# Performance work log

Measured on AMD Instinct MI355X. Metric: run time of the kernel, lower is better.

## Reference

```python
import jax, jax.numpy as jnp
import numpy as np

N_NODES = 50000
N_EDGES = 600000
IN_DIM, H_DIM, OUT_DIM = 128, 128, 64
NUM_RELS = 8


def setup_inputs() -> dict:
    key = jax.random.key(0)
    ks = jax.random.split(key, 10)
    x = jax.random.normal(ks[0], (N_NODES, IN_DIM), dtype=jnp.float32)
    edge_index = jax.random.randint(ks[1], (2, N_EDGES), 0, N_NODES, dtype=jnp.int64 if jax.config.read('jax_enable_x64') else jnp.int32)
    edge_type = jax.random.randint(ks[2], (N_EDGES,), 0, NUM_RELS, dtype=edge_index.dtype)
    s1 = 1.0 / np.sqrt(IN_DIM)
    s2 = 1.0 / np.sqrt(H_DIM)
    W1 = jax.random.uniform(ks[3], (NUM_RELS, IN_DIM, H_DIM), jnp.float32, -s1, s1)
    root1 = jax.random.uniform(ks[4], (IN_DIM, H_DIM), jnp.float32, -s1, s1)
    b1 = jnp.zeros((H_DIM,), jnp.float32)
    W2 = jax.random.uniform(ks[5], (NUM_RELS, H_DIM, OUT_DIM), jnp.float32, -s2, s2)
    root2 = jax.random.uniform(ks[6], (H_DIM, OUT_DIM), jnp.float32, -s2, s2)
    b2 = jnp.zeros((OUT_DIM,), jnp.float32)
    return {"x": x, "edge_index": edge_index, "edge_type": edge_type,
            "W1": W1, "root1": root1, "b1": b1, "W2": W2, "root2": root2, "b2": b2}


def rgcn_conv(x, src, dst, et, W, Wr, b, num_rels):
    # h_i = W_root x_i + b + sum_r (1/|N_r(i)|) sum_{j in N_r(i)} W_r x_j  (mean per relation)
    N = x.shape[0]
    xs = jnp.einsum('ni,rio->rno', x, W)          # [R, N, out]: transform once per relation
    msgs = xs[et, src]                            # [E, out]: gather per-edge transformed source
    seg = dst * num_rels + et                     # combined (dst, rel) segment id
    deg = jax.ops.segment_sum(jnp.ones(et.shape, jnp.float32), seg, num_segments=N * num_rels)
    norm = 1.0 / jnp.maximum(deg[seg], 1.0)       # per-relation in-degree normalization
    agg = jax.ops.segment_sum(msgs * norm[:, None], dst, num_segments=N)
    return agg + x @ Wr + b


def reference(x, edge_index, edge_type, W1, root1, b1, W2, root2, b2):
    src, dst = edge_index[0], edge_index[1]
    h = rgcn_conv(x, src, dst, edge_type, W1, root1, b1, NUM_RELS)
    h = jax.nn.relu(h)
    out = rgcn_conv(h, src, dst, edge_type, W2, root2, b2, NUM_RELS)
    return out
```

## Files before the change

kernel.cpp:

```cpp
#include <hip/hip_runtime.h>

#define NRELS 8

typedef __attribute__((ext_vector_type(8))) short short8;
typedef __attribute__((ext_vector_type(4))) float f32x4;

__device__ __forceinline__ unsigned short f2bf(float f) {
  unsigned int u = __float_as_uint(f);
  u += 0x7FFFu + ((u >> 16) & 1u);
  return (unsigned short)(u >> 16);
}
__device__ __forceinline__ float bf2f(unsigned short h) {
  return __uint_as_float(((unsigned int)h) << 16);
}

__device__ __forceinline__ void gload_lds16(const void* g, void* l) {
  __builtin_amdgcn_global_load_lds(
      (const __attribute__((address_space(1))) unsigned int*)g,
      (__attribute__((address_space(3))) unsigned int*)l, 16, 0, 0);
}


__global__ __launch_bounds__(256) void zero_kernel(int* __restrict__ p, int n) {
  int i = blockIdx.x * blockDim.x + threadIdx.x;
  if (i < n) p[i] = 0;
}


__global__ __launch_bounds__(256) void hist_kernel(
    const int* __restrict__ dstp, const int* __restrict__ et, int E,
    int* __restrict__ hist) {
  int i = blockIdx.x * blockDim.x + threadIdx.x;
  if (i < E) {
    atomicAdd(&hist[(size_t)dstp[i] * NRELS + et[i]], 1);
  }
}


__global__ __launch_bounds__(256) void scan1_kernel(
    const int* __restrict__ hist, int M, int* __restrict__ row_off,
    int* __restrict__ bsum, float* __restrict__ nrm) {
  __shared__ int s[256];
  int t = threadIdx.x;
  int i = blockIdx.x * 256 + t;
  int v = (i < M) ? hist[i] : 0;
  if (i < M) nrm[i] = 1.0f / (float)max(v, 1);
  s[t] = v;
  __syncthreads();
  for (int off = 1; off < 256; off <<= 1) {
    int u = (t >= off) ? s[t - off] : 0;
    __syncthreads();
    s[t] += u;
    __syncthreads();
  }
  if (i < M) row_off[i] = s[t] - v;
  if (t == 255) bsum[blockIdx.x] = s[255];
}

__global__ __launch_bounds__(256) void scan2_kernel(int* __restrict__ bsum, int NB) {
  __shared__ int s[256];
  int t = threadIdx.x;
  int C = (NB + 255) / 256;
  int b0 = t * C, b1 = min(NB, b0 + C);
  int sum = 0;
  for (int i = b0; i < b1; i++) sum += bsum[i];
  s[t] = sum;
  __syncthreads();
  for (int off = 1; off < 256; off <<= 1) {
    int u = (t >= off) ? s[t - off] : 0;
    __syncthreads();
    s[t] += u;
    __syncthreads();
  }
  int base = (t == 0) ? 0 : s[t - 1];
  for (int i = b0; i < b1; i++) {
    int v = bsum[i];
    bsum[i] = base;
    base += v;
  }
  if (t == 255) bsum[NB] = s[255];
}

__global__ __launch_bounds__(256) void scan3_kernel(
    int* __restrict__ row_off, int* __restrict__ cursor,
    const int* __restrict__ bsum, int M, int NB) {
  int i = blockIdx.x * 256 + threadIdx.x;
  if (i < M) {
    int v = row_off[i] + bsum[i >> 8];
    row_off[i] = v;
    cursor[i] = v;
  } else if (i == M) {
    row_off[M] = bsum[NB];
  }
}


__global__ __launch_bounds__(256) void bucket_kernel(
    const int* __restrict__ src, const int* __restrict__ dstp,
    const int* __restrict__ et, int E, int* __restrict__ cursor,
    int* __restrict__ epack) {
  int i = blockIdx.x * blockDim.x + threadIdx.x;
  if (i < E) {
    int r = et[i];
    int pos = atomicAdd(&cursor[(size_t)dstp[i] * NRELS + r], 1);
    epack[pos] = src[i] | (r << 20);
  }
}


__global__ __launch_bounds__(256) void cvt_x_kernel(
    const float* __restrict__ x, unsigned short* __restrict__ xb, int n4) {
  int i = blockIdx.x * blockDim.x + threadIdx.x;
  if (i < n4) {
    float4 v = ((const float4*)x)[i];
    ushort4 o;
    o.x = f2bf(v.x); o.y = f2bf(v.y); o.z = f2bf(v.z); o.w = f2bf(v.w);
    ((ushort4*)xb)[i] = o;
  }
}


__global__ __launch_bounds__(256) void cvt_w_kernel(
    const float* __restrict__ W1, const float* __restrict__ root1,
    const float* __restrict__ W2, const float* __restrict__ root2,
    unsigned short* __restrict__ Bt1, unsigned short* __restrict__ Bt2) {
  int idx = blockIdx.x * blockDim.x + threadIdx.x;
  const int T1 = 1152 * 128;
  const int T2 = 576 * 128;
  if (idx < T1) {
    int n = idx >> 7, k = idx & 127;
    float v;
    if (n < 1024) {
      int r = n >> 7, c = n & 127;
      v = W1[((size_t)r * 128 + k) * 128 + c];
    } else {
      v = root1[(size_t)k * 128 + (n - 1024)];
    }
    Bt1[idx] = f2bf(v);
  } else if (idx < T1 + T2) {
    int j = idx - T1;
    int n = j >> 7, k = j & 127;
    float v;
    if (n < 512) {
      int r = n >> 6, c = n & 63;
      v = W2[((size_t)r * 128 + k) * 64 + c];
    } else {
      v = root2[(size_t)k * 64 + (n - 512)];
    }
    Bt2[j] = f2bf(v);
  }
}


template <int BN, int TILES>
__global__ __launch_bounds__(256) void gemm_xs(
    const unsigned short* __restrict__ A,
    const unsigned short* __restrict__ Bt,
    unsigned short* __restrict__ Cout,
    int N, int NC) {
  constexpr int FM = 2;
  constexpr int FN = BN / 32;

  __shared__ unsigned short As[64 * 128];
  __shared__ unsigned short Bs[BN * 128];

  const int tid = threadIdx.x;
  const int lane = tid & 63;
  const int wid = tid >> 6;
  const int wm = wid >> 1, wn = wid & 1;
  const int l15 = lane & 15, lhi = lane >> 4;
  const int bm0 = blockIdx.y * 64;
  const int ng0 = blockIdx.x * BN * TILES;

#pragma unroll
  for (int c = 0; c < 4; c++) {
    int o = c * 4096 + tid * 16;
    int row = o >> 8;
    int scol = ((o & 255) ^ ((row & 7) << 4)) >> 1;
    int gr = bm0 + row;
    gr = gr < N ? gr : N - 1;
    gload_lds16(A + (size_t)gr * 128 + scol, (char*)As + o);
  }

  for (int t = 0; t < TILES; t++) {
    const int n0 = ng0 + t * BN;
    if (t) __syncthreads();
#pragma unroll
    for (int c = 0; c < BN / 16; c++) {
      int o = c * 4096 + tid * 16;
      int n = o >> 8;
      int scol = ((o & 255) ^ ((n & 7) << 4)) >> 1;
      gload_lds16(Bt + (size_t)(n0 + n) * 128 + scol, (char*)Bs + o);
    }
    asm volatile("s_waitcnt vmcnt(0)" ::: "memory");
    __syncthreads();

    f32x4 acc[FM][FN];
#pragma unroll
    for (int i = 0; i < FM; i++)
#pragma unroll
      for (int j = 0; j < FN; j++) acc[i][j] = (f32x4){0.f, 0.f, 0.f, 0.f};

#pragma unroll
    for (int ks = 0; ks < 4; ks++) {
      short8 af[FM], bf[FN];
#pragma unroll
      for (int fm = 0; fm < FM; fm++) {
        int row = wm * 32 + fm * 16 + l15;
        af[fm] = *(const short8*)((const char*)As + row * 256 +
                                  ((ks * 64 + lhi * 16) ^ ((row & 7) << 4)));
      }
#pragma unroll
      for (int fn = 0; fn < FN; fn++) {
        int n = wn * (BN / 2) + fn * 16 + l15;
        bf[fn] = *(const short8*)((const char*)Bs + n * 256 +
                                  ((ks * 64 + lhi * 16) ^ ((n & 7) << 4)));
      }
#pragma unroll
      for (int fm = 0; fm < FM; fm++)
#pragma unroll
        for (int fn = 0; fn < FN; fn++)
          acc[fm][fn] = __builtin_amdgcn_mfma_f32_16x16x32_bf16(
              af[fm], bf[fn], acc[fm][fn], 0, 0, 0);
    }

#pragma unroll
    for (int fm = 0; fm < FM; fm++) {
#pragma unroll
      for (int fn = 0; fn < FN; fn++) {
        int col = n0 + wn * (BN / 2) + fn * 16 + l15;
#pragma unroll
        for (int i = 0; i < 4; i++) {
          int row = bm0 + wm * 32 + fm * 16 + lhi * 4 + i;
          if (row < N) {
            Cout[(size_t)row * NC + col] = f2bf(acc[fm][fn][i]);
          }
        }
      }
    }
  }
}


__global__ __launch_bounds__(256) void agg_finish1(
    const unsigned short* __restrict__ xs,
    const int* __restrict__ row_off,
    const int* __restrict__ epack,
    const float* __restrict__ nrm,
    const float* __restrict__ b1,
    unsigned short* __restrict__ h,
    int N) {
  int wid = (int)((blockIdx.x * blockDim.x + threadIdx.x) >> 6);
  if (wid >= N) return;
  int lane = threadIdx.x & 63;
  int lo2 = lane * 2;
  unsigned int own = *(const unsigned int*)(xs + (size_t)wid * 1152 + 1024 + lo2);
  float acc0 = bf2f((unsigned short)(own & 0xFFFF)) + b1[lo2];
  float acc1 = bf2f((unsigned short)(own >> 16)) + b1[lo2 + 1];
  int kb = wid * NRELS;
  int b = row_off[kb], e = row_off[kb + NRELS];
  int i = b;
  for (; i + 3 < e; i += 4) {
    int p0 = epack[i], p1 = epack[i + 1], p2 = epack[i + 2], p3 = epack[i + 3];
    unsigned int u0 = *(const unsigned int*)(xs + (size_t)(p0 & 0xFFFFF) * 1152 + ((p0 >> 20) << 7) + lo2);
    unsigned int u1 = *(const unsigned int*)(xs + (size_t)(p1 & 0xFFFFF) * 1152 + ((p1 >> 20) << 7) + lo2);
    unsigned int u2 = *(const unsigned int*)(xs + (size_t)(p2 & 0xFFFFF) * 1152 + ((p2 >> 20) << 7) + lo2);
    unsigned int u3 = *(const unsigned int*)(xs + (size_t)(p3 & 0xFFFFF) * 1152 + ((p3 >> 20) << 7) + lo2);
    float n0 = nrm[kb + (p0 >> 20)], n1 = nrm[kb + (p1 >> 20)];
    float n2 = nrm[kb + (p2 >> 20)], n3 = nrm[kb + (p3 >> 20)];
    acc0 += bf2f((unsigned short)(u0 & 0xFFFF)) * n0 + bf2f((unsigned short)(u1 & 0xFFFF)) * n1 +
            bf2f((unsigned short)(u2 & 0xFFFF)) * n2 + bf2f((unsigned short)(u3 & 0xFFFF)) * n3;
    acc1 += bf2f((unsigned short)(u0 >> 16)) * n0 + bf2f((unsigned short)(u1 >> 16)) * n1 +
            bf2f((unsigned short)(u2 >> 16)) * n2 + bf2f((unsigned short)(u3 >> 16)) * n3;
  }
  for (; i < e; i++) {
    int p = epack[i];
    unsigned int u = *(const unsigned int*)(xs + (size_t)(p & 0xFFFFF) * 1152 + ((p >> 20) << 7) + lo2);
    float nv = nrm[kb + (p >> 20)];
    acc0 += bf2f((unsigned short)(u & 0xFFFF)) * nv;
    acc1 += bf2f((unsigned short)(u >> 16)) * nv;
  }
  unsigned int o = (unsigned int)f2bf(fmaxf(acc0, 0.f)) |
                   ((unsigned int)f2bf(fmaxf(acc1, 0.f)) << 16);
  *(unsigned int*)(h + (size_t)wid * 128 + lo2) = o;
}


__global__ __launch_bounds__(256) void agg_finish2(
    const unsigned short* __restrict__ ys,
    const int* __restrict__ row_off,
    const int* __restrict__ epack,
    const float* __restrict__ nrm,
    const float* __restrict__ b2,
    float* __restrict__ outp,
    int N) {
  int wid = (int)((blockIdx.x * blockDim.x + threadIdx.x) >> 6);
  if (wid >= N) return;
  int col = threadIdx.x & 63;
  float acc = bf2f(ys[(size_t)wid * 576 + 512 + col]) + b2[col];
  int kb = wid * NRELS;
  int b = row_off[kb], e = row_off[kb + NRELS];
  int i = b;
  for (; i + 3 < e; i += 4) {
    int p0 = epack[i], p1 = epack[i + 1], p2 = epack[i + 2], p3 = epack[i + 3];
    float v0 = bf2f(ys[(size_t)(p0 & 0xFFFFF) * 576 + ((p0 >> 20) << 6) + col]);
    float v1 = bf2f(ys[(size_t)(p1 & 0xFFFFF) * 576 + ((p1 >> 20) << 6) + col]);
    float v2 = bf2f(ys[(size_t)(p2 & 0xFFFFF) * 576 + ((p2 >> 20) << 6) + col]);
    float v3 = bf2f(ys[(size_t)(p3 & 0xFFFFF) * 576 + ((p3 >> 20) << 6) + col]);
    acc += v0 * nrm[kb + (p0 >> 20)] + v1 * nrm[kb + (p1 >> 20)] +
           v2 * nrm[kb + (p2 >> 20)] + v3 * nrm[kb + (p3 >> 20)];
  }
  for (; i < e; i++) {
    int p = epack[i];
    acc += bf2f(ys[(size_t)(p & 0xFFFFF) * 576 + ((p >> 20) << 6) + col]) * nrm[kb + (p >> 20)];
  }
  outp[(size_t)wid * 64 + col] = acc;
}


extern "C" void kernel_launch(void* const* d_in, const int* in_sizes, int n_in,
                              void* d_out, int out_size, void* d_ws, size_t ws_size,
                              hipStream_t stream) {
  const float* x     = (const float*)d_in[0];
  const int*   eidx  = (const int*)d_in[1];
  const int*   et    = (const int*)d_in[2];
  const float* W1    = (const float*)d_in[3];
  const float* root1 = (const float*)d_in[4];
  const float* b1    = (const float*)d_in[5];
  const float* W2    = (const float*)d_in[6];
  const float* root2 = (const float*)d_in[7];
  const float* b2    = (const float*)d_in[8];
  float* out = (float*)d_out;

  const int IN = 128;
  const int N = in_sizes[0] / IN;
  const int E = in_sizes[2];
  const int* src = eidx;
  const int* dst = eidx + E;
  const int M = N * NRELS;
  const int NB = (M + 255) / 256;

  auto align = [](size_t v) { return (v + 255) & ~(size_t)255; };
  char* base = (char*)d_ws;
  size_t o = 0;
  int* hist = (int*)(base + o);
  o = align((size_t)M * 4);
  int* row_off = (int*)(base + o);
  o = align(o + (size_t)(M + 1) * 4);
  int* cursor = (int*)(base + o);
  o = align(o + (size_t)M * 4);
  int* bsum = (int*)(base + o);
  o = align(o + (size_t)(NB + 1) * 4);
  float* nrm = (float*)(base + o);
  o = align(o + (size_t)M * 4);
  int* epack = (int*)(base + o);
  o = align(o + (size_t)E * 4);
  unsigned short* xb = (unsigned short*)(base + o);
  o = align(o + (size_t)N * 128 * 2);
  unsigned short* hb = (unsigned short*)(base + o);
  o = align(o + (size_t)N * 128 * 2);
  unsigned short* Bt1 = (unsigned short*)(base + o);
  o = align(o + (size_t)1152 * 128 * 2);
  unsigned short* Bt2 = (unsigned short*)(base + o);
  o = align(o + (size_t)576 * 128 * 2);
  unsigned short* xs = (unsigned short*)(base + o);

  const int tb = 256;
  zero_kernel<<<(M + tb - 1) / tb, tb, 0, stream>>>(hist, M);
  hist_kernel<<<(E + tb - 1) / tb, tb, 0, stream>>>(dst, et, E, hist);
  scan1_kernel<<<NB, 256, 0, stream>>>(hist, M, row_off, bsum, nrm);
  scan2_kernel<<<1, 256, 0, stream>>>(bsum, NB);
  scan3_kernel<<<(M + 256) / 256, 256, 0, stream>>>(row_off, cursor, bsum, M, NB);
  bucket_kernel<<<(E + tb - 1) / tb, tb, 0, stream>>>(src, dst, et, E, cursor, epack);
  cvt_x_kernel<<<(N * 128 / 4 + tb - 1) / tb, tb, 0, stream>>>(x, xb, N * 128 / 4);
  cvt_w_kernel<<<((1152 + 576) * 128 + tb - 1) / tb, tb, 0, stream>>>(
      W1, root1, W2, root2, Bt1, Bt2);

  const int agrid = (N + 3) / 4;
  const int gblocks = (N + 63) / 64;

  {
    dim3 g(3, gblocks);
    gemm_xs<128, 3><<<g, 256, 0, stream>>>(xb, Bt1, xs, N, 1152);
  }
  agg_finish1<<<agrid, 256, 0, stream>>>(xs, row_off, epack, nrm, b1, hb, N);

  {
    dim3 g(3, gblocks);
    gemm_xs<64, 3><<<g, 256, 0, stream>>>(hb, Bt2, xs, N, 576);
  }
  agg_finish2<<<agrid, 256, 0, stream>>>(xs, row_off, epack, nrm, b2, out, N);
}
```

Baseline: 206.8 us.

## Double-buffer B tiles in GEMM, stage output through LDS, unroll gathers by eight

The GEMM now uses a fixed 64-column tile with two LDS B buffers, so the next tile's load overlaps the current tile's MFMA work. Results are written back through swizzled LDS and stored as coalesced 16-byte rows instead of scattered 2-byte stores. The aggregation kernels issue eight gathered loads before accumulating rather than four, which gives more memory parallelism. The cost is extra barriers, more LDS use, and more registers in the gather loops.

New measurement: 216.8 us. 4.9% more time.

```diff
diff --git a/kernel.cpp b/kernel.cpp
--- a/kernel.cpp
+++ b/kernel.cpp
@@ -152,17 +152,16 @@
 }
 
 
-template <int BN, int TILES>
+template <int TILES>
 __global__ __launch_bounds__(256) void gemm_xs(
     const unsigned short* __restrict__ A,
     const unsigned short* __restrict__ Bt,
     unsigned short* __restrict__ Cout,
     int N, int NC) {
-  constexpr int FM = 2;
-  constexpr int FN = BN / 32;
+  constexpr int BN = 64;
 
   __shared__ unsigned short As[64 * 128];
-  __shared__ unsigned short Bs[BN * 128];
+  __shared__ unsigned short Bs[2][64 * 128];
 
   const int tid = threadIdx.x;
   const int lane = tid & 63;
@@ -181,61 +180,89 @@
     gr = gr < N ? gr : N - 1;
     gload_lds16(A + (size_t)gr * 128 + scol, (char*)As + o);
   }
+#pragma unroll
+  for (int c = 0; c < 4; c++) {
+    int o = c * 4096 + tid * 16;
+    int n = o >> 8;
+    int scol = ((o & 255) ^ ((n & 7) << 4)) >> 1;
+    gload_lds16(Bt + (size_t)(ng0 + n) * 128 + scol, (char*)Bs[0] + o);
+  }
 
   for (int t = 0; t < TILES; t++) {
+    const int bb = t & 1;
     const int n0 = ng0 + t * BN;
-    if (t) __syncthreads();
-#pragma unroll
-    for (int c = 0; c < BN / 16; c++) {
-      int o = c * 4096 + tid * 16;
-      int n = o >> 8;
-      int scol = ((o & 255) ^ ((n & 7) << 4)) >> 1;
-      gload_lds16(Bt + (size_t)(n0 + n) * 128 + scol, (char*)Bs + o);
-    }
-    asm volatile("s_waitcnt vmcnt(0)" ::: "memory");
-    __syncthreads();
-
-    f32x4 acc[FM][FN];
-#pragma unroll
-    for (int i = 0; i < FM; i++)
-#pragma unroll
-      for (int j = 0; j < FN; j++) acc[i][j] = (f32x4){0.f, 0.f, 0.f, 0.f};
+    __syncthreads();
+    if (t + 1 < TILES) {
+      const int n1 = n0 + BN;
+#pragma unroll
+      for (int c = 0; c < 4; c++) {
+        int o = c * 4096 + tid * 16;
+        int n = o >> 8;
+        int scol = ((o & 255) ^ ((n & 7) << 4)) >> 1;
+        gload_lds16(Bt + (size_t)(n1 + n) * 128 + scol, (char*)Bs[bb ^ 1] + o);
+      }
+      asm volatile("s_waitcnt vmcnt(4)" ::: "memory");
+    } else {
+      asm volatile("s_waitcnt vmcnt(0)" ::: "memory");
+    }
+    __syncthreads();
+
+    f32x4 acc[2][2];
+#pragma unroll
+    for (int i = 0; i < 2; i++)
+#pragma unroll
+      for (int j = 0; j < 2; j++) acc[i][j] = (f32x4){0.f, 0.f, 0.f, 0.f};
 
 #pragma unroll
     for (int ks = 0; ks < 4; ks++) {
-      short8 af[FM], bf[FN];
-#pragma unroll
-      for (int fm = 0; fm < FM; fm++) {
+      short8 af[2], bf[2];
+#pragma unroll
+      for (int fm = 0; fm < 2; fm++) {
         int row = wm * 32 + fm * 16 + l15;
         af[fm] = *(const short8*)((const char*)As + row * 256 +
                                   ((ks * 64 + lhi * 16) ^ ((row & 7) << 4)));
       }
 #pragma unroll
-      for (int fn = 0; fn < FN; fn++) {
-        int n = wn * (BN / 2) + fn * 16 + l15;
-        bf[fn] = *(const short8*)((const char*)Bs + n * 256 +
+      for (int fn = 0; fn < 2; fn++) {
+        int n = wn * 32 + fn * 16 + l15;
+        bf[fn] = *(const short8*)((const char*)Bs[bb] + n * 256 +
                                   ((ks * 64 + lhi * 16) ^ ((n & 7) << 4)));
       }
 #pragma unroll
-      for (int fm = 0; fm < FM; fm++)
-#pragma unroll
-        for (int fn = 0; fn < FN; fn++)
+      for (int fm = 0; fm < 2; fm++)
+#pragma unroll
+        for (int fn = 0; fn < 2; fn++)
           acc[fm][fn] = __builtin_amdgcn_mfma_f32_16x16x32_bf16(
               af[fm], bf[fn], acc[fm][fn], 0, 0, 0);
     }
 
-#pragma unroll
-    for (int fm = 0; fm < FM; fm++) {
-#pragma unroll
-      for (int fn = 0; fn < FN; fn++) {
-        int col = n0 + wn * (BN / 2) + fn * 16 + l15;
+    __syncthreads();
+
+#pragma unroll
+    for (int fm = 0; fm < 2; fm++) {
+#pragma unroll
+      for (int fn = 0; fn < 2; fn++) {
+        int col = wn * 32 + fn * 16 + l15;
 #pragma unroll
         for (int i = 0; i < 4; i++) {
-          int row = bm0 + wm * 32 + fm * 16 + lhi * 4 + i;
-          if (row < N) {
-            Cout[(size_t)row * NC + col] = f2bf(acc[fm][fn][i]);
-          }
+          int row = wm * 32 + fm * 16 + lhi * 4 + i;
+          int byte = (row * 128 + col * 2) ^ ((row & 7) << 4);
+          *(unsigned short*)((char*)Bs[bb] + byte) = f2bf(acc[fm][fn][i]);
         }
+      }
+    }
+    __syncthreads();
+
+#pragma unroll
+    for (int j = 0; j < 2; j++) {
+      int flat = j * 4096 + tid * 16;
+      int row = flat >> 7;
+      int k16 = flat & 127;
+      int grow = bm0 + row;
+      if (grow < N) {
+        short8 v = *(const short8*)((const char*)Bs[bb] + row * 128 +
+                                    (k16 ^ ((row & 7) << 4)));
+        *(short8*)((char*)(Cout + (size_t)grow * NC + n0) + k16) = v;
       }
     }
   }
@@ -260,18 +287,20 @@
   int kb = wid * NRELS;
   int b = row_off[kb], e = row_off[kb + NRELS];
   int i = b;
-  for (; i + 3 < e; i += 4) {
-    int p0 = epack[i], p1 = epack[i + 1], p2 = epack[i + 2], p3 = epack[i + 3];
-    unsigned int u0 = *(const unsigned int*)(xs + (size_t)(p0 & 0xFFFFF) * 1152 + ((p0 >> 20) << 7) + lo2);
-    unsigned int u1 = *(const unsigned int*)(xs + (size_t)(p1 & 0xFFFFF) * 1152 + ((p1 >> 20) << 7) + lo2);
-    unsigned int u2 = *(const unsigned int*)(xs + (size_t)(p2 & 0xFFFFF) * 1152 + ((p2 >> 20) << 7) + lo2);
-    unsigned int u3 = *(const unsigned int*)(xs + (size_t)(p3 & 0xFFFFF) * 1152 + ((p3 >> 20) << 7) + lo2);
-    float n0 = nrm[kb + (p0 >> 20)], n1 = nrm[kb + (p1 >> 20)];
-    float n2 = nrm[kb + (p2 >> 20)], n3 = nrm[kb + (p3 >> 20)];
-    acc0 += bf2f((unsigned short)(u0 & 0xFFFF)) * n0 + bf2f((unsigned short)(u1 & 0xFFFF)) * n1 +
-            bf2f((unsigned short)(u2 & 0xFFFF)) * n2 + bf2f((unsigned short)(u3 & 0xFFFF)) * n3;
-    acc1 += bf2f((unsigned short)(u0 >> 16)) * n0 + bf2f((unsigned short)(u1 >> 16)) * n1 +
-            bf2f((unsigned short)(u2 >> 16)) * n2 + bf2f((unsigned short)(u3 >> 16)) * n3;
+  for (; i + 7 < e; i += 8) {
+    unsigned int u[8];
+    float nv[8];
+#pragma unroll
+    for (int q = 0; q < 8; q++) {
+      int p = epack[i + q];
+      u[q] = *(const unsigned int*)(xs + (size_t)(p & 0xFFFFF) * 1152 + ((p >> 20) << 7) + lo2);
+      nv[q] = nrm[kb + (p >> 20)];
+    }
+#pragma unroll
+    for (int q = 0; q < 8; q++) {
+      acc0 += bf2f((unsigned short)(u[q] & 0xFFFF)) * nv[q];
+      acc1 += bf2f((unsigned short)(u[q] >> 16)) * nv[q];
+    }
   }
   for (; i < e; i++) {
     int p = epack[i];
@@ -301,14 +330,16 @@
   int kb = wid * NRELS;
   int b = row_off[kb], e = row_off[kb + NRELS];
   int i = b;
-  for (; i + 3 < e; i += 4) {
-    int p0 = epack[i], p1 = epack[i + 1], p2 = epack[i + 2], p3 = epack[i + 3];
-    float v0 = bf2f(ys[(size_t)(p0 & 0xFFFFF) * 576 + ((p0 >> 20) << 6) + col]);
-    float v1 = bf2f(ys[(size_t)(p1 & 0xFFFFF) * 576 + ((p1 >> 20) << 6) + col]);
-    float v2 = bf2f(ys[(size_t)(p2 & 0xFFFFF) * 576 + ((p2 >> 20) << 6) + col]);
-    float v3 = bf2f(ys[(size_t)(p3 & 0xFFFFF) * 576 + ((p3 >> 20) << 6) + col]);
-    acc += v0 * nrm[kb + (p0 >> 20)] + v1 * nrm[kb + (p1 >> 20)] +
-           v2 * nrm[kb + (p2 >> 20)] + v3 * nrm[kb + (p3 >> 20)];
+  for (; i + 7 < e; i += 8) {
+    float v[8], nv[8];
+#pragma unroll
+    for (int q = 0; q < 8; q++) {
+      int p = epack[i + q];
+      v[q] = bf2f(ys[(size_t)(p & 0xFFFFF) * 576 + ((p >> 20) << 6) + col]);
+      nv[q] = nrm[kb + (p >> 20)];
+    }
+#pragma unroll
+    for (int q = 0; q < 8; q++) acc += v[q] * nv[q];
   }
   for (; i < e; i++) {
     int p = epack[i];
@@ -381,13 +412,13 @@
 
   {
     dim3 g(3, gblocks);
-    gemm_xs<128, 3><<<g, 256, 0, stream>>>(xb, Bt1, xs, N, 1152);
+    gemm_xs<6><<<g, 256, 0, stream>>>(xb, Bt1, xs, N, 1152);
   }
   agg_finish1<<<agrid, 256, 0, stream>>>(xs, row_off, epack, nrm, b1, hb, N);
 
   {
     dim3 g(3, gblocks);
-    gemm_xs<64, 3><<<g, 256, 0, stream>>>(hb, Bt2, xs, N, 576);
+    gemm_xs<3><<<g, 256, 0, stream>>>(hb, Bt2, xs, N, 576);
   }
   agg_finish2<<<agrid, 256, 0, stream>>>(xs, row_off, epack, nrm, b2, out, N);
 }
```
